# Optimization experiments

Measured on AMD Instinct MI355X. Metric: run time of the kernel, lower is better.

Reference implementation:

```python
import jax, jax.numpy as jnp
import numpy as np

T, B, IN_DIM = 2048, 8, 512
D_VALUE, D_KEY = 512, 128
CHUNK = 128
EPS = 1e-8


def setup_inputs() -> dict:
    key = jax.random.key(0)
    ks = jax.random.split(key, 9)
    s = 0.02
    return {
        "x": jax.random.normal(ks[0], (T, B, IN_DIM), dtype=jnp.float32),
        "Wv": jax.random.normal(ks[1], (D_VALUE, IN_DIM), dtype=jnp.float32) * s,
        "bv": jnp.zeros((D_VALUE,), dtype=jnp.float32),
        "Wk": jax.random.normal(ks[2], (D_KEY, IN_DIM), dtype=jnp.float32) * s,
        "bk": jnp.zeros((D_KEY,), dtype=jnp.float32),
        "Wq": jax.random.normal(ks[3], (D_KEY, IN_DIM), dtype=jnp.float32) * s,
        "bq": jnp.zeros((D_KEY,), dtype=jnp.float32),
        "Wa": jax.random.normal(ks[4], (D_KEY, IN_DIM), dtype=jnp.float32) * s,
        "ba": jnp.zeros((D_KEY,), dtype=jnp.float32),
    }


def _gla_forward(x, Wv, bv, Wk, bk, Wq, bq, Wa, ba):
    # Projections: x (T,B,in) -> v (T,B,d), k/q/alpha (T,B,n)
    v = jnp.einsum("tbi,di->tbd", x, Wv) + bv
    k = jnp.einsum("tbi,ni->tbn", x, Wk) + bk
    q = jnp.einsum("tbi,ni->tbn", x, Wq) + bq
    alpha = jax.nn.sigmoid(jnp.einsum("tbi,ni->tbn", x, Wa) + ba)

    Tt, Bb, d = v.shape
    n = k.shape[2]
    nch = Tt // CHUNK  # T chosen divisible by CHUNK

    # Reshape time-major tensors into (n_chunks, C, B, dim)
    v_r = v.reshape(nch, CHUNK, Bb, d)
    k_r = k.reshape(nch, CHUNK, Bb, n)
    q_r = q.reshape(nch, CHUNK, Bb, n)
    a_r = alpha.reshape(nch, CHUNK, Bb, n)

    def chunk_step(S_prev, inp):
        v_ch, k_ch, q_ch, a_ch = inp  # (C,B,d), (C,B,n), (C,B,n), (C,B,n)
        outer = jnp.einsum("tbd,tbn->tbdn", v_ch, k_ch)  # (C,B,d,n)
        cp = jnp.cumprod(jnp.maximum(a_ch, EPS), axis=0)  # (C,B,n)
        inv_prefix = 1.0 / (cp + EPS)
        scaled = jnp.cumsum(outer * inv_prefix[:, :, None, :], axis=0)
        # local decayed state plus carried state decayed by prefix product
        S_local = (scaled + S_prev[None, :, :, :]) * cp[:, :, None, :]
        y_ch = jnp.einsum("tbdn,tbn->tbd", S_local, q_ch)  # S @ q
        return S_local[-1], y_ch

    S0 = jnp.zeros((Bb, d, n), dtype=v.dtype)
    _, y = jax.lax.scan(chunk_step, S0, (v_r, k_r, q_r, a_r))
    return y.reshape(Tt, Bb, d)


def reference(x, Wv, bv, Wk, bk, Wq, bq, Wa, ba):
    return _gla_forward(x, Wv, bv, Wk, bk, Wq, bq, Wa, ba)
```

## Files before the change

### kernel.cpp

```cpp
#include <hip/hip_runtime.h>


#define EPSV 1e-8f

typedef __bf16 bf16x8 __attribute__((ext_vector_type(8)));
typedef float f32x4 __attribute__((ext_vector_type(4)));

__device__ __forceinline__ void async_copy16(const void* g, void* l) {
  __builtin_amdgcn_global_load_lds(
      (const __attribute__((address_space(1))) void*)g,
      (__attribute__((address_space(3))) void*)l, 16, 0, 0);
}

__global__ __launch_bounds__(256) void conv_bf16(const float* __restrict__ src,
                                                 __bf16* __restrict__ dst) {
  long i = ((long)blockIdx.x * 256 + threadIdx.x) * 8;
  float4 f0 = *(const float4*)(src + i);
  float4 f1 = *(const float4*)(src + i + 4);
  bf16x8 h;
  h[0] = (__bf16)f0.x; h[1] = (__bf16)f0.y; h[2] = (__bf16)f0.z; h[3] = (__bf16)f0.w;
  h[4] = (__bf16)f1.x; h[5] = (__bf16)f1.y; h[6] = (__bf16)f1.z; h[7] = (__bf16)f1.w;
  *(bf16x8*)(dst + i) = h;
}

__global__ __launch_bounds__(256) void conv_w(const float* __restrict__ Wv,
                                              const float* __restrict__ Wk,
                                              const float* __restrict__ Wq,
                                              const float* __restrict__ Wa,
                                              __bf16* __restrict__ dst) {
  long i = ((long)blockIdx.x * 256 + threadIdx.x) * 8;
  int row = (int)(i >> 9);
  int col = (int)(i & 511);
  const float* src;
  if (row < 512)      src = Wv + (long)row * 512 + col;
  else if (row < 640) src = Wk + (long)(row - 512) * 512 + col;
  else if (row < 768) src = Wq + (long)(row - 640) * 512 + col;
  else                src = Wa + (long)(row - 768) * 512 + col;
  float4 f0 = *(const float4*)(src);
  float4 f1 = *(const float4*)(src + 4);
  bf16x8 h;
  h[0] = (__bf16)f0.x; h[1] = (__bf16)f0.y; h[2] = (__bf16)f0.z; h[3] = (__bf16)f0.w;
  h[4] = (__bf16)f1.x; h[5] = (__bf16)f1.y; h[6] = (__bf16)f1.z; h[7] = (__bf16)f1.w;
  *(bf16x8*)(dst + i) = h;
}

__global__ __launch_bounds__(256) void proj_mfma(
    const __bf16* __restrict__ xb, const __bf16* __restrict__ wcat,
    const float* __restrict__ bv, const float* __restrict__ bk,
    const float* __restrict__ bq, const float* __restrict__ ba,
    __bf16* __restrict__ vt, __bf16* __restrict__ kout,
    __bf16* __restrict__ qout, float* __restrict__ aout) {
  __shared__ __attribute__((aligned(16))) char smem[128 * 136 * 2];
  __bf16* a_sm = (__bf16*)smem;
  __bf16* b_sm = a_sm + 128 * 32;
  __bf16* tr   = (__bf16*)smem;

  int tid = threadIdx.x;
  int lane = tid & 63, wave = tid >> 6;
  int mt = blockIdx.x, nt = blockIdx.y;
  int wr = wave >> 1, wcol = wave & 1;

  const __bf16* xtile = xb + (long)mt * 128 * 512;
  const __bf16* wtile = wcat + (long)nt * 128 * 512;

  f32x4 acc[4][4] = {};
  int lr = lane >> 2, lc = lane & 3;
  int l15 = lane & 15, qd = lane >> 4;

  for (int k0 = 0; k0 < 512; k0 += 32) {
#pragma unroll
    for (int h = 0; h < 2; ++h) {
      int q = wave * 2 + h;
      int row = q * 16 + lr;
      async_copy16(xtile + (long)row * 512 + k0 + lc * 8, &a_sm[q * 512]);
      async_copy16(wtile + (long)row * 512 + k0 + lc * 8, &b_sm[q * 512]);
    }
    __syncthreads();
    bf16x8 af[4], bfr[4];
#pragma unroll
    for (int t = 0; t < 4; ++t) {
      af[t]  = *(const bf16x8*)&a_sm[(wr * 64 + t * 16 + l15) * 32 + qd * 8];
      bfr[t] = *(const bf16x8*)&b_sm[(wcol * 64 + t * 16 + l15) * 32 + qd * 8];
    }
#pragma unroll
    for (int i = 0; i < 4; ++i)
#pragma unroll
      for (int j = 0; j < 4; ++j)
        acc[i][j] = __builtin_amdgcn_mfma_f32_16x16x32_bf16(af[i], bfr[j], acc[i][j], 0, 0, 0);
    __syncthreads();
  }

  if (nt < 4) {
    const float* bias = bv + nt * 128;
#pragma unroll
    for (int i = 0; i < 4; ++i)
#pragma unroll
      for (int j = 0; j < 4; ++j) {
        int col = wcol * 64 + j * 16 + l15;
        float bz = bias[col];
#pragma unroll
        for (int r = 0; r < 4; ++r) {
          int row = wr * 64 + i * 16 + qd * 4 + r;
          tr[col * 136 + (row & 7) * 16 + (row >> 3)] = (__bf16)(acc[i][j][r] + bz);
        }
      }
    __syncthreads();
    int cbase = (mt >> 3) * 8;
    int s0 = (mt & 7) * 16;
#pragma unroll
    for (int it = 0; it < 4; ++it) {
      int p = it * 256 + tid;
      int d = p & 127, b = p >> 7;
      bf16x8 u0 = *(const bf16x8*)&tr[d * 136 + b * 16];
      bf16x8 u1 = *(const bf16x8*)&tr[d * 136 + b * 16 + 8];
      __bf16* dst = vt + ((long)(cbase + b) * 512 + nt * 128 + d) * 128 + s0;
      *(bf16x8*)dst = u0;
      *(bf16x8*)(dst + 8) = u1;
    }
    return;
  }

  const float* bias; bool sig = false;
  __bf16* dstb = nullptr; float* dstf = nullptr;
  if (nt == 4)      { bias = bk; dstb = kout; }
  else if (nt == 5) { bias = bq; dstb = qout; }
  else              { bias = ba; dstf = aout; sig = true; }

#pragma unroll
  for (int i = 0; i < 4; ++i)
#pragma unroll
    for (int j = 0; j < 4; ++j) {
      int col = wcol * 64 + j * 16 + l15;
      float bz = bias[col];
#pragma unroll
      for (int r = 0; r < 4; ++r) {
        int row = wr * 64 + i * 16 + qd * 4 + r;
        float z = acc[i][j][r] + bz;
        long addr = ((long)mt * 128 + row) * 128 + col;
        if (sig) dstf[addr] = 1.f / (1.f + __expf(-z));
        else     dstb[addr] = (__bf16)z;
      }
    }
}

__global__ __launch_bounds__(256) void scan_cp(const float* __restrict__ a,
                                               const __bf16* __restrict__ k,
                                               const __bf16* __restrict__ q,
                                               __bf16* __restrict__ kbs,
                                               __bf16* __restrict__ qb,
                                               __bf16* __restrict__ kt,
                                               float* __restrict__ cpend) {
  int idx = blockIdx.x * 256 + threadIdx.x;
  int n = idx & 127;
  int b = (idx >> 7) & 7;
  int c = idx >> 10;
  long base = ((long)c * 1024 + b) * 128 + n;
  float cp = 1.f;
  __bf16 ktbuf[128];
#pragma unroll
  for (int tt = 0; tt < 128; ++tt) {
    long off = base + (long)tt * 1024;
    float av = fmaxf(a[off], EPSV);
    cp *= av;
    float kk = (float)k[off] / (cp + EPSV);
    float qq = (float)q[off] * cp;
    __bf16 kh = (__bf16)kk;
    kbs[off] = kh;
    qb[off] = (__bf16)qq;
    ktbuf[tt] = kh;
  }
  cpend[(c * 8 + b) * 128 + n] = cp;
  __bf16* dst = kt + ((long)((c * 8 + b) * 128 + n)) * 128;
#pragma unroll
  for (int i = 0; i < 16; ++i) {
    bf16x8 h;
#pragma unroll
    for (int j = 0; j < 8; ++j) h[j] = ktbuf[i * 8 + j];
    *(bf16x8*)(dst + i * 8) = h;
  }
}

__global__ __launch_bounds__(256) void gmm(const __bf16* __restrict__ vt,
                                           const __bf16* __restrict__ kt,
                                           const float* __restrict__ cpend,
                                           __bf16* __restrict__ Gt) {
  int tid = threadIdx.x, lane = tid & 63, wave = tid >> 6;
  int wr = wave >> 1, wc = wave & 1;
  int l15 = lane & 15, qd = lane >> 4;
  int cb = blockIdx.x >> 2, dt = blockIdx.x & 3;
  const __bf16* vbase = vt + ((long)cb * 512 + dt * 128) * 128;
  const __bf16* kbase = kt + (long)cb * 16384;
  f32x4 acc[4][4] = {};
#pragma unroll
  for (int kk = 0; kk < 4; ++kk) {
    int k0 = kk * 32;
    bf16x8 af[4], bfr[4];
#pragma unroll
    for (int i = 0; i < 4; ++i)
      af[i] = *(const bf16x8*)(vbase + (long)(wr * 64 + i * 16 + l15) * 128 + k0 + qd * 8);
#pragma unroll
    for (int j = 0; j < 4; ++j)
      bfr[j] = *(const bf16x8*)(kbase + (long)(wc * 64 + j * 16 + l15) * 128 + k0 + qd * 8);
#pragma unroll
    for (int i = 0; i < 4; ++i)
#pragma unroll
      for (int j = 0; j < 4; ++j)
        acc[i][j] = __builtin_amdgcn_mfma_f32_16x16x32_bf16(af[i], bfr[j], acc[i][j], 0, 0, 0);
  }
  float ce[4];
#pragma unroll
  for (int j = 0; j < 4; ++j) ce[j] = cpend[cb * 128 + wc * 64 + j * 16 + l15];
#pragma unroll
  for (int i = 0; i < 4; ++i)
#pragma unroll
    for (int j = 0; j < 4; ++j) {
      int col = wc * 64 + j * 16 + l15;
#pragma unroll
      for (int r = 0; r < 4; ++r) {
        int row = wr * 64 + i * 16 + qd * 4 + r;
        Gt[((long)cb * 512 + dt * 128 + row) * 128 + col] = (__bf16)(acc[i][j][r] * ce[j]);
      }
    }
}

__global__ __launch_bounds__(256) void scan_state(const __bf16* __restrict__ Gt,
                                                  const float* __restrict__ cpend,
                                                  __bf16* __restrict__ St) {
  long e = (long)blockIdx.x * 256 + threadIdx.x;
  int n = (int)(e & 127);
  int b = (int)(e >> 16);
  float S = 0.f;
#pragma unroll
  for (int c = 0; c < 16; ++c) {
    long idx = (long)c * 524288 + e;
    float g = (float)Gt[idx];
    St[idx] = (__bf16)S;
    S = g + S * cpend[(c * 8 + b) * 128 + n];
  }
}

__global__ __launch_bounds__(256) void ymm(const __bf16* __restrict__ qb,
                                           const __bf16* __restrict__ kbs,
                                           const __bf16* __restrict__ vt,
                                           const __bf16* __restrict__ St,
                                           float* __restrict__ out) {
  __shared__ __bf16 A_lds[128 * 136];
  int tid = threadIdx.x, lane = tid & 63, wave = tid >> 6;
  int wr = wave >> 1, wc = wave & 1;
  int l15 = lane & 15, qd = lane >> 4;
  int cb = blockIdx.x >> 2, dt = blockIdx.x & 3;
  int c = cb >> 3, b = cb & 7;
  const __bf16* qbase = qb + ((long)c * 1024 + b) * 128;
  const __bf16* kbase = kbs + ((long)c * 1024 + b) * 128;

  {
    f32x4 accA[4][4] = {};
#pragma unroll
    for (int kk = 0; kk < 4; ++kk) {
      int k0 = kk * 32;
      bf16x8 af[4], bfr[4];
#pragma unroll
      for (int i = 0; i < 4; ++i)
        af[i] = *(const bf16x8*)(qbase + (long)(wr * 64 + i * 16 + l15) * 1024 + k0 + qd * 8);
#pragma unroll
      for (int j = 0; j < 4; ++j)
        bfr[j] = *(const bf16x8*)(kbase + (long)(wc * 64 + j * 16 + l15) * 1024 + k0 + qd * 8);
#pragma unroll
      for (int i = 0; i < 4; ++i)
#pragma unroll
        for (int j = 0; j < 4; ++j)
          accA[i][j] = __builtin_amdgcn_mfma_f32_16x16x32_bf16(af[i], bfr[j], accA[i][j], 0, 0, 0);
    }
#pragma unroll
    for (int i = 0; i < 4; ++i)
#pragma unroll
      for (int j = 0; j < 4; ++j) {
        int s = wc * 64 + j * 16 + l15;
#pragma unroll
        for (int r = 0; r < 4; ++r) {
          int t = wr * 64 + i * 16 + qd * 4 + r;
          A_lds[t * 136 + s] = (s <= t) ? (__bf16)accA[i][j][r] : (__bf16)0.f;
        }
      }
  }
  __syncthreads();

  f32x4 acc[4][4] = {};
  const __bf16* vbase = vt + ((long)cb * 512 + dt * 128) * 128;
  const __bf16* sbase = St + ((long)cb * 512 + dt * 128) * 128;
#pragma unroll
  for (int kk = 0; kk < 4; ++kk) {
    int k0 = kk * 32;
    bf16x8 af[4], bfr[4];
#pragma unroll
    for (int i = 0; i < 4; ++i)
      af[i] = *(const bf16x8*)(vbase + (long)(wr * 64 + i * 16 + l15) * 128 + k0 + qd * 8);
#pragma unroll
    for (int j = 0; j < 4; ++j)
      bfr[j] = *(const bf16x8*)&A_lds[(wc * 64 + j * 16 + l15) * 136 + k0 + qd * 8];
#pragma unroll
    for (int i = 0; i < 4; ++i)
#pragma unroll
      for (int j = 0; j < 4; ++j)
        acc[i][j] = __builtin_amdgcn_mfma_f32_16x16x32_bf16(af[i], bfr[j], acc[i][j], 0, 0, 0);
  }
#pragma unroll
  for (int kk = 0; kk < 4; ++kk) {
    int k0 = kk * 32;
    bf16x8 af[4], bfr[4];
#pragma unroll
    for (int i = 0; i < 4; ++i)
      af[i] = *(const bf16x8*)(sbase + (long)(wr * 64 + i * 16 + l15) * 128 + k0 + qd * 8);
#pragma unroll
    for (int j = 0; j < 4; ++j)
      bfr[j] = *(const bf16x8*)(qbase + (long)(wc * 64 + j * 16 + l15) * 1024 + k0 + qd * 8);
#pragma unroll
    for (int i = 0; i < 4; ++i)
#pragma unroll
      for (int j = 0; j < 4; ++j)
        acc[i][j] = __builtin_amdgcn_mfma_f32_16x16x32_bf16(af[i], bfr[j], acc[i][j], 0, 0, 0);
  }

#pragma unroll
  for (int i = 0; i < 4; ++i)
#pragma unroll
    for (int j = 0; j < 4; ++j) {
      int colt = wc * 64 + j * 16 + l15;
      long addr = ((long)(c * 128 + colt) * 8 + b) * 512 + dt * 128 + wr * 64 + i * 16 + qd * 4;
      *(float4*)(out + addr) = *(float4*)&acc[i][j];
    }
}

extern "C" void kernel_launch(void* const* d_in, const int* in_sizes, int n_in,
                              void* d_out, int out_size, void* d_ws, size_t ws_size,
                              hipStream_t stream) {
  const float* x  = (const float*)d_in[0];
  const float* Wv = (const float*)d_in[1];
  const float* bv = (const float*)d_in[2];
  const float* Wk = (const float*)d_in[3];
  const float* bk = (const float*)d_in[4];
  const float* Wq = (const float*)d_in[5];
  const float* bq = (const float*)d_in[6];
  const float* Wa = (const float*)d_in[7];
  const float* ba = (const float*)d_in[8];
  float* out = (float*)d_out;
  float* ws = (float*)d_ws;

  float*  a_buf = ws;
  __bf16* qb    = (__bf16*)(ws + 2097152);
  __bf16* kbs   = (__bf16*)(ws + 3145728);
  __bf16* kt    = (__bf16*)(ws + 4194304);
  __bf16* vt    = (__bf16*)(ws + 5242880);
  __bf16* k_raw = (__bf16*)(ws + 9437184);
  __bf16* q_raw = (__bf16*)(ws + 10485760);
  __bf16* xb    = (__bf16*)(ws + 11534336);
  __bf16* Wcat  = (__bf16*)(ws + 15728640);
  __bf16* Gt    = xb;
  __bf16* St    = (__bf16*)(ws + 15958016);
  float*  cpend = ws + 20152320;

  conv_bf16<<<4096, 256, 0, stream>>>(x, xb);
  conv_w<<<224, 256, 0, stream>>>(Wv, Wk, Wq, Wa, Wcat);
  proj_mfma<<<dim3(128, 7), 256, 0, stream>>>(xb, Wcat, bv, bk, bq, ba,
                                              vt, k_raw, q_raw, a_buf);
  scan_cp<<<64, 256, 0, stream>>>(a_buf, k_raw, q_raw, kbs, qb, kt, cpend);
  gmm<<<512, 256, 0, stream>>>(vt, kt, cpend, Gt);
  scan_state<<<2048, 256, 0, stream>>>(Gt, cpend, St);
  ymm<<<512, 256, 0, stream>>>(qb, kbs, vt, St, out);
}
```

Measured before the change: 200.2 us.

## Merge conversion kernels, drop LDS staging in projection GEMM, split scan blocks

Merges the x and weight bf16 conversion kernels into one launch. The projection GEMM now loads MFMA operand fragments straight from global memory instead of staging them through LDS with barriers, which removes the per-k synchronisation but issues uncoalesced, partly redundant global loads. The chunk scan uses 128 blocks of 128 threads instead of 64 of 256, and computes a reciprocal where it used to divide, which gives more parallel blocks for a latency-bound serial loop.

```diff
diff --git a/kernel.cpp b/kernel.cpp
--- a/kernel.cpp
+++ b/kernel.cpp
@@ -6,42 +6,36 @@
 typedef __bf16 bf16x8 __attribute__((ext_vector_type(8)));
 typedef float f32x4 __attribute__((ext_vector_type(4)));
 
-__device__ __forceinline__ void async_copy16(const void* g, void* l) {
-  __builtin_amdgcn_global_load_lds(
-      (const __attribute__((address_space(1))) void*)g,
-      (__attribute__((address_space(3))) void*)l, 16, 0, 0);
-}
-
-__global__ __launch_bounds__(256) void conv_bf16(const float* __restrict__ src,
-                                                 __bf16* __restrict__ dst) {
-  long i = ((long)blockIdx.x * 256 + threadIdx.x) * 8;
-  float4 f0 = *(const float4*)(src + i);
-  float4 f1 = *(const float4*)(src + i + 4);
-  bf16x8 h;
-  h[0] = (__bf16)f0.x; h[1] = (__bf16)f0.y; h[2] = (__bf16)f0.z; h[3] = (__bf16)f0.w;
-  h[4] = (__bf16)f1.x; h[5] = (__bf16)f1.y; h[6] = (__bf16)f1.z; h[7] = (__bf16)f1.w;
-  *(bf16x8*)(dst + i) = h;
-}
-
-__global__ __launch_bounds__(256) void conv_w(const float* __restrict__ Wv,
-                                              const float* __restrict__ Wk,
-                                              const float* __restrict__ Wq,
-                                              const float* __restrict__ Wa,
-                                              __bf16* __restrict__ dst) {
-  long i = ((long)blockIdx.x * 256 + threadIdx.x) * 8;
-  int row = (int)(i >> 9);
-  int col = (int)(i & 511);
-  const float* src;
-  if (row < 512)      src = Wv + (long)row * 512 + col;
-  else if (row < 640) src = Wk + (long)(row - 512) * 512 + col;
-  else if (row < 768) src = Wq + (long)(row - 640) * 512 + col;
-  else                src = Wa + (long)(row - 768) * 512 + col;
-  float4 f0 = *(const float4*)(src);
-  float4 f1 = *(const float4*)(src + 4);
-  bf16x8 h;
-  h[0] = (__bf16)f0.x; h[1] = (__bf16)f0.y; h[2] = (__bf16)f0.z; h[3] = (__bf16)f0.w;
-  h[4] = (__bf16)f1.x; h[5] = (__bf16)f1.y; h[6] = (__bf16)f1.z; h[7] = (__bf16)f1.w;
-  *(bf16x8*)(dst + i) = h;
+__global__ __launch_bounds__(256) void conv_all(
+    const float* __restrict__ x,
+    const float* __restrict__ Wv, const float* __restrict__ Wk,
+    const float* __restrict__ Wq, const float* __restrict__ Wa,
+    __bf16* __restrict__ xb, __bf16* __restrict__ wcat) {
+  int bid = blockIdx.x;
+  if (bid < 4096) {
+    long i = ((long)bid * 256 + threadIdx.x) * 8;
+    float4 f0 = *(const float4*)(x + i);
+    float4 f1 = *(const float4*)(x + i + 4);
+    bf16x8 h;
+    h[0] = (__bf16)f0.x; h[1] = (__bf16)f0.y; h[2] = (__bf16)f0.z; h[3] = (__bf16)f0.w;
+    h[4] = (__bf16)f1.x; h[5] = (__bf16)f1.y; h[6] = (__bf16)f1.z; h[7] = (__bf16)f1.w;
+    *(bf16x8*)(xb + i) = h;
+  } else {
+    long i = ((long)(bid - 4096) * 256 + threadIdx.x) * 8;
+    int row = (int)(i >> 9);
+    int col = (int)(i & 511);
+    const float* src;
+    if (row < 512)      src = Wv + (long)row * 512 + col;
+    else if (row < 640) src = Wk + (long)(row - 512) * 512 + col;
+    else if (row < 768) src = Wq + (long)(row - 640) * 512 + col;
+    else                src = Wa + (long)(row - 768) * 512 + col;
+    float4 f0 = *(const float4*)(src);
+    float4 f1 = *(const float4*)(src + 4);
+    bf16x8 h;
+    h[0] = (__bf16)f0.x; h[1] = (__bf16)f0.y; h[2] = (__bf16)f0.z; h[3] = (__bf16)f0.w;
+    h[4] = (__bf16)f1.x; h[5] = (__bf16)f1.y; h[6] = (__bf16)f1.z; h[7] = (__bf16)f1.w;
+    *(bf16x8*)(wcat + i) = h;
+  }
 }
 
 __global__ __launch_bounds__(256) void proj_mfma(
@@ -50,44 +44,32 @@
     const float* __restrict__ bq, const float* __restrict__ ba,
     __bf16* __restrict__ vt, __bf16* __restrict__ kout,
     __bf16* __restrict__ qout, float* __restrict__ aout) {
-  __shared__ __attribute__((aligned(16))) char smem[128 * 136 * 2];
-  __bf16* a_sm = (__bf16*)smem;
-  __bf16* b_sm = a_sm + 128 * 32;
-  __bf16* tr   = (__bf16*)smem;
+  __shared__ __bf16 tr[128 * 136];
 
   int tid = threadIdx.x;
   int lane = tid & 63, wave = tid >> 6;
   int mt = blockIdx.x, nt = blockIdx.y;
   int wr = wave >> 1, wcol = wave & 1;
-
-  const __bf16* xtile = xb + (long)mt * 128 * 512;
-  const __bf16* wtile = wcat + (long)nt * 128 * 512;
+  int l15 = lane & 15, qd = lane >> 4;
+
+  const __bf16* abase = xb + ((long)mt * 128 + wr * 64) * 512;
+  const __bf16* bbase = wcat + ((long)nt * 128 + wcol * 64) * 512;
 
   f32x4 acc[4][4] = {};
-  int lr = lane >> 2, lc = lane & 3;
-  int l15 = lane & 15, qd = lane >> 4;
-
+#pragma unroll 4
   for (int k0 = 0; k0 < 512; k0 += 32) {
-#pragma unroll
-    for (int h = 0; h < 2; ++h) {
-      int q = wave * 2 + h;
-      int row = q * 16 + lr;
-      async_copy16(xtile + (long)row * 512 + k0 + lc * 8, &a_sm[q * 512]);
-      async_copy16(wtile + (long)row * 512 + k0 + lc * 8, &b_sm[q * 512]);
-    }
-    __syncthreads();
     bf16x8 af[4], bfr[4];
 #pragma unroll
-    for (int t = 0; t < 4; ++t) {
-      af[t]  = *(const bf16x8*)&a_sm[(wr * 64 + t * 16 + l15) * 32 + qd * 8];
-      bfr[t] = *(const bf16x8*)&b_sm[(wcol * 64 + t * 16 + l15) * 32 + qd * 8];
-    }
+    for (int i = 0; i < 4; ++i)
+      af[i] = *(const bf16x8*)(abase + (long)(i * 16 + l15) * 512 + k0 + qd * 8);
+#pragma unroll
+    for (int j = 0; j < 4; ++j)
+      bfr[j] = *(const bf16x8*)(bbase + (long)(j * 16 + l15) * 512 + k0 + qd * 8);
 #pragma unroll
     for (int i = 0; i < 4; ++i)
 #pragma unroll
       for (int j = 0; j < 4; ++j)
         acc[i][j] = __builtin_amdgcn_mfma_f32_16x16x32_bf16(af[i], bfr[j], acc[i][j], 0, 0, 0);
-    __syncthreads();
   }
 
   if (nt < 4) {
@@ -143,34 +125,34 @@
     }
 }
 
-__global__ __launch_bounds__(256) void scan_cp(const float* __restrict__ a,
+__global__ __launch_bounds__(128) void scan_cp(const float* __restrict__ a,
                                                const __bf16* __restrict__ k,
                                                const __bf16* __restrict__ q,
                                                __bf16* __restrict__ kbs,
                                                __bf16* __restrict__ qb,
                                                __bf16* __restrict__ kt,
                                                float* __restrict__ cpend) {
-  int idx = blockIdx.x * 256 + threadIdx.x;
-  int n = idx & 127;
-  int b = (idx >> 7) & 7;
-  int c = idx >> 10;
+  int n = threadIdx.x;
+  int blk = blockIdx.x;
+  int b = blk & 7, c = blk >> 3;
   long base = ((long)c * 1024 + b) * 128 + n;
   float cp = 1.f;
   __bf16 ktbuf[128];
 #pragma unroll
   for (int tt = 0; tt < 128; ++tt) {
     long off = base + (long)tt * 1024;
-    float av = fmaxf(a[off], EPSV);
-    cp *= av;
-    float kk = (float)k[off] / (cp + EPSV);
-    float qq = (float)q[off] * cp;
-    __bf16 kh = (__bf16)kk;
+    float av = a[off];
+    float kv = (float)k[off];
+    float qv = (float)q[off];
+    cp *= fmaxf(av, EPSV);
+    float inv = 1.f / (cp + EPSV);
+    __bf16 kh = (__bf16)(kv * inv);
     kbs[off] = kh;
-    qb[off] = (__bf16)qq;
+    qb[off] = (__bf16)(qv * cp);
     ktbuf[tt] = kh;
   }
-  cpend[(c * 8 + b) * 128 + n] = cp;
-  __bf16* dst = kt + ((long)((c * 8 + b) * 128 + n)) * 128;
+  cpend[blk * 128 + n] = cp;
+  __bf16* dst = kt + ((long)(blk * 128 + n)) * 128;
 #pragma unroll
   for (int i = 0; i < 16; ++i) {
     bf16x8 h;
@@ -359,11 +341,10 @@
   __bf16* St    = (__bf16*)(ws + 15958016);
   float*  cpend = ws + 20152320;
 
-  conv_bf16<<<4096, 256, 0, stream>>>(x, xb);
-  conv_w<<<224, 256, 0, stream>>>(Wv, Wk, Wq, Wa, Wcat);
+  conv_all<<<4320, 256, 0, stream>>>(x, Wv, Wk, Wq, Wa, xb, Wcat);
   proj_mfma<<<dim3(128, 7), 256, 0, stream>>>(xb, Wcat, bv, bk, bq, ba,
                                               vt, k_raw, q_raw, a_buf);
-  scan_cp<<<64, 256, 0, stream>>>(a_buf, k_raw, q_raw, kbs, qb, kt, cpend);
+  scan_cp<<<128, 128, 0, stream>>>(a_buf, k_raw, q_raw, kbs, qb, kt, cpend);
   gmm<<<512, 256, 0, stream>>>(vt, kt, cpend, Gt);
   scan_state<<<2048, 256, 0, stream>>>(Gt, cpend, St);
   ymm<<<512, 256, 0, stream>>>(qb, kbs, vt, St, out);
```

Result: slower. 238.6 us (+19.2%).
